# Kernel tuning notes

Hardware: AMD Instinct MI355X
Metric: run time of the kernel (lower is better)

Reference implementation:

```python
import jax, jax.numpy as jnp
import numpy as np
from itertools import permutations, combinations

BATCH = 32768
EPS = 1e-06  # positivity eps from __init__


def _levi_civita7():
    e = np.zeros((7,) * 7, dtype=np.float32)
    for p in permutations(range(7)):
        inv = sum(1 for i in range(7) for j in range(i + 1, 7) if p[i] > p[j])
        e[p] = -1.0 if inv % 2 else 1.0
    return jnp.asarray(e)

_EPS7 = _levi_civita7()  # (7,7,7,7,7,7,7) rank-7 Levi-Civita tensor
_TRIPLES = np.array(list(combinations(range(7), 3)), dtype=np.int32)  # (35,3) i<j<k index triples
_PERMS3 = [((0, 1, 2), 1.0), ((1, 2, 0), 1.0), ((2, 0, 1), 1.0),
           ((0, 2, 1), -1.0), ((2, 1, 0), -1.0), ((1, 0, 2), -1.0)]


def _phi_full(phi):
    # expand 35 independent components to fully antisymmetric (B,7,7,7)
    b = phi.shape[0]
    pf = jnp.zeros((b, 7, 7, 7), phi.dtype)
    for perm, s in _PERMS3:
        ia = _TRIPLES[:, perm[0]]
        ib = _TRIPLES[:, perm[1]]
        ic = _TRIPLES[:, perm[2]]
        pf = pf.at[:, ia, ib, ic].set(s * phi)
    return pf


def _metric_from_phi(phi):
    # Standard G2 metric: B_ij = (1/144) phi_ikl phi_jmn phi_pqr eps^{klmnpqr};
    # g = B / |det B|^{1/9}  (unit-determinant normalization)
    pf = _phi_full(phi)  # (B,7,7,7)
    C = jnp.einsum('klmnpqr,bpqr->bklmn', _EPS7, pf)  # (B,7,7,7,7)
    T = jnp.einsum('bklmn,bjmn->bklj', C, pf)          # (B,7,7,7)
    Bm = jnp.einsum('bikl,bklj->bij', pf, T) / 144.0   # (B,7,7)
    det = jnp.linalg.det(Bm)
    g = Bm / (jnp.abs(det)[:, None, None] + 1e-12) ** (1.0 / 9.0)
    return 0.5 * (g + jnp.swapaxes(g, -1, -2))  # exact symmetry for eigvalsh


def setup_inputs() -> dict:
    key = jax.random.key(0)
    phi = jax.random.normal(key, (BATCH, 35), dtype=jnp.float32)
    return {"phi": phi}


def reference(phi):
    g = _metric_from_phi(phi)              # (B,7,7)
    ev = jnp.linalg.eigvalsh(g)            # (B,7)
    return jax.nn.relu(-ev + EPS).sum(axis=-1)  # (B,) sum of negative-eigenvalue violations
```

## Files before the change

kernel.cpp:

```cpp
#include <hip/hip_runtime.h>
#include <utility>

#define BATCH 32768
#define NPHI 35

constexpr int choose2(int n){ return (n*(n-1))/2; }

constexpr int tri_id_sorted(int a,int b,int c){
  int id=0;
  for(int x=0;x<a;++x) id += choose2(6-x);
  for(int y=a+1;y<b;++y) id += (6-y);
  id += (c-b-1);
  return id;
}

constexpr int tri_id3(int a,int b,int c){
  int x=a,y=b,z=c;
  if (x>y){int t=x;x=y;y=t;}
  if (y>z){int t=y;y=z;z=t;}
  if (x>y){int t=x;x=y;y=t;}
  return tri_id_sorted(x,y,z);
}

constexpr int sgn3(int a,int b,int c){
  int inv = (a>b)+(a>c)+(b>c);
  return (inv&1)? -1 : 1;
}

constexpr int UT(int i,int j){
  return i*7 - (i*(i-1))/2 + (j-i);
}

constexpr int PAIR(int k,int l){
  return k*7 - (k*(k+1))/2 + (l - k - 1);
}

struct Prog {
  int n;
  unsigned char kind[1472];
  unsigned char init[1472];
  short         dst [1472];
  unsigned char a   [1472];
  short         b   [1472];
  signed char   s   [1472];
};

constexpr Prog build_prog(){
  Prog P{}; P.n=0;
  bool uinit[28]={};
  for(int k=0;k<7;++k) for(int l=k+1;l<7;++l){
    const int kl = PAIR(k,l);
    bool tinit[7]={};
    for(int m=0;m<7;++m) for(int n2=m+1;n2<7;++n2){
      if(m==k||m==l||n2==k||n2==l) continue;
      int comp[3]={0,0,0}; int cn=0;
      for(int x=0;x<7;++x) if(x!=k&&x!=l&&x!=m&&x!=n2){ comp[cn]=x; ++cn; }
      int perm[7]={k,l,m,n2,comp[0],comp[1],comp[2]};
      int invc=0;
      for(int i=0;i<7;++i) for(int j=i+1;j<7;++j) if(perm[i]>perm[j]) ++invc;
      const int es=(invc&1)? -1 : 1;
      const int tcomp=tri_id_sorted(comp[0],comp[1],comp[2]);
      for(int j=0;j<7;++j){
        if(j==m||j==n2) continue;
        P.kind[P.n]=0;
        P.init[P.n]=tinit[j]?0:1; tinit[j]=true;
        P.dst [P.n]=(short)(kl*7+j);
        P.a   [P.n]=(unsigned char)tcomp;
        P.b   [P.n]=(short)tri_id3(j,m,n2);
        P.s   [P.n]=(signed char)(es*sgn3(j,m,n2));
        ++P.n;
      }
    }
    for(int i=0;i<7;++i){
      if(i==k||i==l) continue;
      for(int j=i;j<7;++j){
        P.kind[P.n]=1;
        P.init[P.n]=uinit[UT(i,j)]?0:1; uinit[UT(i,j)]=true;
        P.dst [P.n]=(short)UT(i,j);
        P.a   [P.n]=(unsigned char)tri_id3(i,k,l);
        P.b   [P.n]=(short)(kl*7+j);
        P.s   [P.n]=(signed char)sgn3(i,k,l);
        ++P.n;
      }
    }
  }
  return P;
}

static constexpr Prog PROG = build_prog();
static_assert(PROG.n == 1470, "program size unexpected");

template<int Q>
__device__ __forceinline__ void step(float (&T)[147], float (&U)[28],
                                     const float (&ph)[NPHI]){
  constexpr int  d = PROG.dst[Q];
  constexpr int  a = PROG.a[Q];
  constexpr int  b = PROG.b[Q];
  constexpr bool neg  = (PROG.s[Q] < 0);
  constexpr bool init = (PROG.init[Q] != 0);
  if constexpr (PROG.kind[Q] == 0){
    const float x = neg ? -ph[a] : ph[a];
    if constexpr (init) T[d] = x * ph[b];
    else                T[d] = fmaf(x, ph[b], T[d]);
  } else {
    const float x = neg ? -ph[a] : ph[a];
    if constexpr (init) U[d] = x * T[b];
    else                U[d] = fmaf(x, T[b], U[d]);
  }
}

template<int... Q>
__device__ __forceinline__ void run_prog(float (&T)[147], float (&U)[28],
                                         const float (&ph)[NPHI],
                                         std::integer_sequence<int, Q...>){
  (step<Q>(T, U, ph), ...);
}

__global__ __launch_bounds__(64,1)
void PositivityConstraint_89086211654295_kernel(const float* __restrict__ phi,
                                                float* __restrict__ out){
  const int gid = blockIdx.x*64 + threadIdx.x;

  const float* __restrict__ p = phi + (size_t)gid * NPHI;
  float ph[NPHI];
  #pragma unroll
  for (int i=0;i<NPHI;++i) ph[i] = p[i];

  float T[147];
  float U[28];
  run_prog(T, U, ph, std::make_integer_sequence<int, PROG.n>{});

  float A[28];
  #pragma unroll
  for (int i=0;i<28;++i) A[i] = U[i]*(1.0f/6.0f);

  for (int sweep=0; sweep<6; ++sweep){
    #pragma unroll
    for (int p1=0;p1<7;++p1){
      #pragma unroll
      for (int q1=p1+1;q1<7;++q1){
        const float apq = A[UT(p1,q1)];
        const float app = A[UT(p1,p1)];
        const float aqq = A[UT(q1,q1)];
        float d = 2.0f*apq;
        d = d + ((d >= 0.0f)? 1e-30f : -1e-30f);
        const float tau = (aqq - app) * __builtin_amdgcn_rcpf(d);
        float t = __builtin_amdgcn_rcpf(
                    fabsf(tau) + __builtin_amdgcn_sqrtf(fmaf(tau,tau,1.0f)));
        t = (tau >= 0.0f)? t : -t;
        const float c = __builtin_amdgcn_rsqf(fmaf(t,t,1.0f));
        const float s = t*c;
        A[UT(p1,p1)] = fmaf(-t, apq, app);
        A[UT(q1,q1)] = fmaf( t, apq, aqq);
        A[UT(p1,q1)] = 0.0f;
        #pragma unroll
        for (int r=0;r<7;++r){
          if (r==p1 || r==q1) continue;
          const int irp = (r<p1)? UT(r,p1) : UT(p1,r);
          const int irq = (r<q1)? UT(r,q1) : UT(q1,r);
          const float arp = A[irp], arq = A[irq];
          A[irp] = fmaf(c, arp, -s*arq);
          A[irq] = fmaf(s, arp,  c*arq);
        }
      }
    }
  }

  float det = 1.0f;
  #pragma unroll
  for (int i=0;i<7;++i) det *= A[UT(i,i)];
  const float ad = fabsf(det) + 1e-12f;
  const float scale = __builtin_amdgcn_exp2f(__builtin_amdgcn_logf(ad) * (1.0f/9.0f));
  const float inv = __builtin_amdgcn_rcpf(scale);

  float sum = 0.0f;
  #pragma unroll
  for (int i=0;i<7;++i){
    const float ev = A[UT(i,i)]*inv;
    const float r = 1e-6f - ev;
    sum += fmaxf(r, 0.0f);
  }
  out[gid] = sum;
}

extern "C" void kernel_launch(void* const* d_in, const int* in_sizes, int n_in,
                              void* d_out, int out_size, void* d_ws, size_t ws_size,
                              hipStream_t stream) {
  const float* phi = (const float*)d_in[0];
  float* out = (float*)d_out;
  (void)in_sizes; (void)n_in; (void)out_size; (void)d_ws; (void)ws_size;
  hipLaunchKernelGGL(PositivityConstraint_89086211654295_kernel,
                     dim3(BATCH/64), dim3(64), 0, stream, phi, out);
}
```

Measured before the change: 65.08 us.

## Group metric contraction per index pair to shrink live temporaries

Restructures the compile-time contraction program so each (k,l) pair computes a 7-element T slice and immediately folds it into the 28-entry symmetric accumulator, instead of materialising a 147-element T array before the second stage. Scheduling barriers between groups are meant to keep register pressure low and avoid spills. The Jacobi rotation angle computation is also reformulated to drop one reciprocal, using a sqrt of s2^2+h^2 instead. That changes rounding slightly and relies on a tiny epsilon to avoid division by zero.

```diff
diff --git a/kernel.cpp b/kernel.cpp
--- a/kernel.cpp
+++ b/kernel.cpp
@@ -3,6 +3,7 @@
 
 #define BATCH 32768
 #define NPHI 35
+#define SWEEPS 6
 
 constexpr int choose2(int n){ return (n*(n-1))/2; }
 
@@ -31,89 +32,102 @@
   return i*7 - (i*(i-1))/2 + (j-i);
 }
 
-constexpr int PAIR(int k,int l){
-  return k*7 - (k*(k+1))/2 + (l - k - 1);
-}
-
-struct Prog {
-  int n;
-  unsigned char kind[1472];
-  unsigned char init[1472];
-  short         dst [1472];
-  unsigned char a   [1472];
-  short         b   [1472];
-  signed char   s   [1472];
+constexpr int pair_k(int g){
+  int idx=0;
+  for(int k=0;k<7;++k) for(int l=k+1;l<7;++l){ if(idx==g) return k; ++idx; }
+  return 0;
+}
+constexpr int pair_l(int g){
+  int idx=0;
+  for(int k=0;k<7;++k) for(int l=k+1;l<7;++l){ if(idx==g) return l; ++idx; }
+  return 0;
+}
+
+struct GProg {
+  int nt, nb;
+  signed char t_dst[50], t_a[50], t_b[50], t_s[50]; unsigned char t_init[50];
+  signed char b_dst[26], b_a[26], b_b[26], b_s[26];
 };
 
-constexpr Prog build_prog(){
-  Prog P{}; P.n=0;
-  bool uinit[28]={};
-  for(int k=0;k<7;++k) for(int l=k+1;l<7;++l){
-    const int kl = PAIR(k,l);
-    bool tinit[7]={};
-    for(int m=0;m<7;++m) for(int n2=m+1;n2<7;++n2){
-      if(m==k||m==l||n2==k||n2==l) continue;
-      int comp[3]={0,0,0}; int cn=0;
-      for(int x=0;x<7;++x) if(x!=k&&x!=l&&x!=m&&x!=n2){ comp[cn]=x; ++cn; }
-      int perm[7]={k,l,m,n2,comp[0],comp[1],comp[2]};
-      int invc=0;
-      for(int i=0;i<7;++i) for(int j=i+1;j<7;++j) if(perm[i]>perm[j]) ++invc;
-      const int es=(invc&1)? -1 : 1;
-      const int tcomp=tri_id_sorted(comp[0],comp[1],comp[2]);
-      for(int j=0;j<7;++j){
-        if(j==m||j==n2) continue;
-        P.kind[P.n]=0;
-        P.init[P.n]=tinit[j]?0:1; tinit[j]=true;
-        P.dst [P.n]=(short)(kl*7+j);
-        P.a   [P.n]=(unsigned char)tcomp;
-        P.b   [P.n]=(short)tri_id3(j,m,n2);
-        P.s   [P.n]=(signed char)(es*sgn3(j,m,n2));
-        ++P.n;
-      }
+constexpr GProg build_group(int k,int l){
+  GProg P{}; P.nt=0; P.nb=0;
+  bool tinit[7]={};
+  for(int m=0;m<7;++m) for(int n2=m+1;n2<7;++n2){
+    if(m==k||m==l||n2==k||n2==l) continue;
+    int comp[3]={0,0,0}; int cn=0;
+    for(int x=0;x<7;++x) if(x!=k&&x!=l&&x!=m&&x!=n2){ comp[cn]=x; ++cn; }
+    int perm[7]={k,l,m,n2,comp[0],comp[1],comp[2]};
+    int invc=0;
+    for(int i=0;i<7;++i) for(int j=i+1;j<7;++j) if(perm[i]>perm[j]) ++invc;
+    const int es=(invc&1)? -1 : 1;
+    const int tcomp=tri_id_sorted(comp[0],comp[1],comp[2]);
+    for(int j=0;j<7;++j){
+      if(j==m||j==n2) continue;
+      P.t_dst[P.nt]=(signed char)j;
+      P.t_a [P.nt]=(signed char)tcomp;
+      P.t_b [P.nt]=(signed char)tri_id3(j,m,n2);
+      P.t_s [P.nt]=(signed char)(es*sgn3(j,m,n2));
+      P.t_init[P.nt]=tinit[j]?0:1; tinit[j]=true;
+      ++P.nt;
     }
-    for(int i=0;i<7;++i){
-      if(i==k||i==l) continue;
-      for(int j=i;j<7;++j){
-        P.kind[P.n]=1;
-        P.init[P.n]=uinit[UT(i,j)]?0:1; uinit[UT(i,j)]=true;
-        P.dst [P.n]=(short)UT(i,j);
-        P.a   [P.n]=(unsigned char)tri_id3(i,k,l);
-        P.b   [P.n]=(short)(kl*7+j);
-        P.s   [P.n]=(signed char)sgn3(i,k,l);
-        ++P.n;
-      }
+  }
+  for(int i=0;i<7;++i){
+    if(i==k||i==l) continue;
+    for(int j=i;j<7;++j){
+      P.b_dst[P.nb]=(signed char)UT(i,j);
+      P.b_a [P.nb]=(signed char)tri_id3(i,k,l);
+      P.b_b [P.nb]=(signed char)j;
+      P.b_s [P.nb]=(signed char)sgn3(i,k,l);
+      ++P.nb;
     }
   }
   return P;
 }
 
-static constexpr Prog PROG = build_prog();
-static_assert(PROG.n == 1470, "program size unexpected");
-
-template<int Q>
-__device__ __forceinline__ void step(float (&T)[147], float (&U)[28],
-                                     const float (&ph)[NPHI]){
-  constexpr int  d = PROG.dst[Q];
-  constexpr int  a = PROG.a[Q];
-  constexpr int  b = PROG.b[Q];
-  constexpr bool neg  = (PROG.s[Q] < 0);
-  constexpr bool init = (PROG.init[Q] != 0);
-  if constexpr (PROG.kind[Q] == 0){
-    const float x = neg ? -ph[a] : ph[a];
-    if constexpr (init) T[d] = x * ph[b];
-    else                T[d] = fmaf(x, ph[b], T[d]);
-  } else {
-    const float x = neg ? -ph[a] : ph[a];
-    if constexpr (init) U[d] = x * T[b];
-    else                U[d] = fmaf(x, T[b], U[d]);
-  }
-}
-
-template<int... Q>
-__device__ __forceinline__ void run_prog(float (&T)[147], float (&U)[28],
-                                         const float (&ph)[NPHI],
-                                         std::integer_sequence<int, Q...>){
-  (step<Q>(T, U, ph), ...);
+template<int G> inline constexpr GProg GP = build_group(pair_k(G), pair_l(G));
+
+template<int G,int Q>
+__device__ __forceinline__ void t_step(float (&T)[7], const float (&ph)[NPHI]){
+  constexpr int d=GP<G>.t_dst[Q], a=GP<G>.t_a[Q], b=GP<G>.t_b[Q];
+  constexpr bool neg=(GP<G>.t_s[Q]<0), ini=(GP<G>.t_init[Q]!=0);
+  const float x = neg ? -ph[a] : ph[a];
+  if constexpr (ini) T[d] = x*ph[b];
+  else               T[d] = fmaf(x, ph[b], T[d]);
+}
+
+template<int G,int Q>
+__device__ __forceinline__ void b_step(float (&U)[28], const float (&T)[7],
+                                       const float (&ph)[NPHI]){
+  constexpr int d=GP<G>.b_dst[Q], a=GP<G>.b_a[Q], b=GP<G>.b_b[Q];
+  constexpr bool neg=(GP<G>.b_s[Q]<0);
+  const float x = neg ? -ph[a] : ph[a];
+  U[d] = fmaf(x, T[b], U[d]);
+}
+
+template<int G,int... TQ>
+__device__ __forceinline__ void run_t(float (&T)[7], const float (&ph)[NPHI],
+                                      std::integer_sequence<int,TQ...>){
+  (t_step<G,TQ>(T,ph), ...);
+}
+template<int G,int... BQ>
+__device__ __forceinline__ void run_b(float (&U)[28], const float (&T)[7],
+                                      const float (&ph)[NPHI],
+                                      std::integer_sequence<int,BQ...>){
+  (b_step<G,BQ>(U,T,ph), ...);
+}
+
+template<int G>
+__device__ __forceinline__ void do_group(float (&U)[28], const float (&ph)[NPHI]){
+  float T[7];
+  run_t<G>(T, ph, std::make_integer_sequence<int, GP<G>.nt>{});
+  run_b<G>(U, T, ph, std::make_integer_sequence<int, GP<G>.nb>{});
+  __builtin_amdgcn_sched_barrier(0);
+}
+
+template<int... G>
+__device__ __forceinline__ void all_groups(float (&U)[28], const float (&ph)[NPHI],
+                                           std::integer_sequence<int,G...>){
+  (do_group<G>(U,ph), ...);
 }
 
 __global__ __launch_bounds__(64,1)
@@ -126,15 +140,17 @@
   #pragma unroll
   for (int i=0;i<NPHI;++i) ph[i] = p[i];
 
-  float T[147];
   float U[28];
-  run_prog(T, U, ph, std::make_integer_sequence<int, PROG.n>{});
+  #pragma unroll
+  for (int i=0;i<28;++i) U[i]=0.f;
+
+  all_groups(U, ph, std::make_integer_sequence<int,21>{});
 
   float A[28];
   #pragma unroll
   for (int i=0;i<28;++i) A[i] = U[i]*(1.0f/6.0f);
 
-  for (int sweep=0; sweep<6; ++sweep){
+  for (int sweep=0; sweep<SWEEPS; ++sweep){
     #pragma unroll
     for (int p1=0;p1<7;++p1){
       #pragma unroll
@@ -142,25 +158,27 @@
         const float apq = A[UT(p1,q1)];
         const float app = A[UT(p1,p1)];
         const float aqq = A[UT(q1,q1)];
-        float d = 2.0f*apq;
-        d = d + ((d >= 0.0f)? 1e-30f : -1e-30f);
-        const float tau = (aqq - app) * __builtin_amdgcn_rcpf(d);
-        float t = __builtin_amdgcn_rcpf(
-                    fabsf(tau) + __builtin_amdgcn_sqrtf(fmaf(tau,tau,1.0f)));
-        t = (tau >= 0.0f)? t : -t;
+        const float s2  = apq + apq;
+        const float h   = aqq - app;
+        const float w   = fmaf(s2, s2, h*h);
+        const float r   = __builtin_amdgcn_sqrtf(w);
+        const float den = fabsf(h) + r + 1e-38f;
+        const float rc  = __builtin_amdgcn_rcpf(den);
+        float t = s2 * rc;
+        t = (h < 0.0f) ? -t : t;
         const float c = __builtin_amdgcn_rsqf(fmaf(t,t,1.0f));
         const float s = t*c;
         A[UT(p1,p1)] = fmaf(-t, apq, app);
         A[UT(q1,q1)] = fmaf( t, apq, aqq);
         A[UT(p1,q1)] = 0.0f;
         #pragma unroll
-        for (int r=0;r<7;++r){
-          if (r==p1 || r==q1) continue;
-          const int irp = (r<p1)? UT(r,p1) : UT(p1,r);
-          const int irq = (r<q1)? UT(r,q1) : UT(q1,r);
+        for (int r2=0;r2<7;++r2){
+          if (r2==p1 || r2==q1) continue;
+          const int irp = (r2<p1)? UT(r2,p1) : UT(p1,r2);
+          const int irq = (r2<q1)? UT(r2,q1) : UT(q1,r2);
           const float arp = A[irp], arq = A[irq];
-          A[irp] = fmaf(c, arp, -s*arq);
-          A[irq] = fmaf(s, arp,  c*arq);
+          A[irp] = fmaf(c, arp, -(s*arq));
+          A[irq] = fmaf(c, arq,  (s*arp));
         }
       }
     }
@@ -177,8 +195,7 @@
   #pragma unroll
   for (int i=0;i<7;++i){
     const float ev = A[UT(i,i)]*inv;
-    const float r = 1e-6f - ev;
-    sum += fmaxf(r, 0.0f);
+    sum += fmaxf(1e-6f - ev, 0.0f);
   }
   out[gid] = sum;
 }
```

After: 65.83 us. No clear change (+1.1%).
